# Optimization experiments

Measured on AMD Instinct MI355X. Metric: run time of the kernel, lower is better.

## Reference

```python
import jax, jax.numpy as jnp
import numpy as np

N, D, H, DH, DFF, E = 4096, 512, 8, 64, 2048, 65536


def setup_inputs() -> dict:
    key = jax.random.key(0)
    ks = jax.random.split(key, 20)
    g = lambda k, s: jax.random.normal(k, s, dtype=jnp.float32) * 0.02
    inp = {
        'x': jax.random.normal(ks[0], (N, D), dtype=jnp.float32),
        'edge_index': jax.random.randint(ks[1], (2, E), 0, N),
        'edge_attr': jax.random.uniform(ks[2], (E,), dtype=jnp.float32),
        'Wg': g(ks[3], (D, D)), 'bg': jnp.zeros((D,), jnp.float32),
        'ln1_s': jnp.ones((D,), jnp.float32), 'ln1_b': jnp.zeros((D,), jnp.float32),
        'Wq': g(ks[4], (D, D)), 'bq': jnp.zeros((D,), jnp.float32),
        'Wk': g(ks[5], (D, D)), 'bk': jnp.zeros((D,), jnp.float32),
        'Wv': g(ks[6], (D, D)), 'bv': jnp.zeros((D,), jnp.float32),
        'Wo': g(ks[7], (D, D)), 'bo': jnp.zeros((D,), jnp.float32),
        'ln2_s': jnp.ones((D,), jnp.float32), 'ln2_b': jnp.zeros((D,), jnp.float32),
        'W1': g(ks[8], (D, DFF)), 'b1': jnp.zeros((DFF,), jnp.float32),
        'W2': g(ks[9], (DFF, D)), 'b2': jnp.zeros((D,), jnp.float32),
        'Wa': g(ks[10], (2 * D, D)), 'ba': jnp.zeros((D,), jnp.float32),
    }
    return inp


def _ln(x, s, b):
    m = x.mean(-1, keepdims=True)
    v = ((x - m) ** 2).mean(-1, keepdims=True)
    return (x - m) * jax.lax.rsqrt(v + 1e-5) * s + b


def _gcn(x, edge_index, ew, Wg, bg):
    # GCNConv: linear, add self-loops (weight 1), sym deg normalization, scatter-add
    xt = x @ Wg                                   # [N, D]
    src = jnp.concatenate([edge_index[0], jnp.arange(N)])
    dst = jnp.concatenate([edge_index[1], jnp.arange(N)])
    w = jnp.concatenate([ew, jnp.ones((N,), ew.dtype)])
    deg = jax.ops.segment_sum(w, dst, num_segments=N)
    dinv = jnp.where(deg > 0, jax.lax.rsqrt(jnp.maximum(deg, 1e-12)), 0.0)
    coef = dinv[src] * w * dinv[dst]              # [E+N]
    out = jax.ops.segment_sum(xt[src] * coef[:, None], dst, num_segments=N)
    return out + bg


def _tfm(x, p):
    # pre-LN vanilla transformer block over all N nodes as one sequence
    h = _ln(x, p['ln1_s'], p['ln1_b'])
    q = (h @ p['Wq'] + p['bq']).reshape(N, H, DH)
    k = (h @ p['Wk'] + p['bk']).reshape(N, H, DH)
    v = (h @ p['Wv'] + p['bv']).reshape(N, H, DH)
    scores = jnp.einsum('nhd,mhd->hnm', q, k) / np.sqrt(DH)
    a = jax.nn.softmax(scores, axis=-1)
    o = jnp.einsum('hnm,mhd->nhd', a, v).reshape(N, D)
    x = x + o @ p['Wo'] + p['bo']
    h2 = _ln(x, p['ln2_s'], p['ln2_b'])
    mlp = jax.nn.gelu(h2 @ p['W1'] + p['b1']) @ p['W2'] + p['b2']
    return x + mlp


def reference(x, edge_index, edge_attr, Wg, bg, ln1_s, ln1_b, Wq, bq, Wk, bk, Wv, bv,
              Wo, bo, ln2_s, ln2_b, W1, b1, W2, b2, Wa, ba):
    p = dict(ln1_s=ln1_s, ln1_b=ln1_b, Wq=Wq, bq=bq, Wk=Wk, bk=bk, Wv=Wv, bv=bv,
             Wo=Wo, bo=bo, ln2_s=ln2_s, ln2_b=ln2_b, W1=W1, b1=b1, W2=W2, b2=b2)
    mp = _gcn(x, edge_index, edge_attr, Wg, bg)
    tf = _tfm(x, p)
    return x + jnp.concatenate([mp, tf], axis=-1) @ Wa + ba
```

## Files before the change

### kernel.cpp

```cpp
#include <hip/hip_runtime.h>
#include <math.h>

#define N_NODES 4096
#define DMODEL  512
#define NHEAD   8
#define DHEAD   64
#define DFF     2048
#define NEDGE   65536
#define QKVLD   1536

typedef unsigned short u16;
typedef __bf16 bf16x8 __attribute__((ext_vector_type(8)));
typedef float  f32x4  __attribute__((ext_vector_type(4)));
typedef short  s16x4  __attribute__((ext_vector_type(4)));

#if defined(__has_builtin)
#if __has_builtin(__builtin_amdgcn_mfma_f32_16x16x16bf16_1k)
#define HAS_MFMA_1K 1
#endif
#endif

__device__ inline float fast_exp2(float x) {
    return __builtin_amdgcn_exp2f(x);
}

__device__ inline f32x4 mfma16(bf16x8 a, bf16x8 b, f32x4 c) {
    return __builtin_amdgcn_mfma_f32_16x16x32_bf16(a, b, c, 0, 0, 0);
}

#ifdef HAS_MFMA_1K
__device__ inline f32x4 mfma1k(s16x4 a, s16x4 b, f32x4 c) {
    return __builtin_amdgcn_mfma_f32_16x16x16bf16_1k(a, b, c, 0, 0, 0);
}
__device__ inline s16x4 pack_bf4(f32x4 p) {
    union { float f; unsigned u; } a0, a1, a2, a3;
    a0.f = p[0]; a1.f = p[1]; a2.f = p[2]; a3.f = p[3];
    unsigned lo = __builtin_amdgcn_perm(a1.u + 0x8000u, a0.u + 0x8000u, 0x07060302u);
    unsigned hi = __builtin_amdgcn_perm(a3.u + 0x8000u, a2.u + 0x8000u, 0x07060302u);
    union { unsigned u[2]; s16x4 v; } r;
    r.u[0] = lo; r.u[1] = hi;
    return r.v;
}
#endif

__device__ inline u16 f2bf(float f) {
    union { float f; unsigned u; } v; v.f = f;
    unsigned r = v.u + 0x7fff + ((v.u >> 16) & 1);
    return (u16)(r >> 16);
}

__device__ inline float bf2f(u16 v) {
    union { unsigned u; float f; } t; t.u = ((unsigned)v) << 16; return t.f;
}

__device__ inline float gelu_tanh(float x) {
    float x3 = x * x * x;
    float t = tanhf(0.7978845608028654f * (x + 0.044715f * x3));
    return 0.5f * x * (1.0f + t);
}

#define GBN 128
#define GBK 32
#define GP  40

template <int ACT, int OBF16>
__launch_bounds__(512)
__global__ void mfma_gemm64(const u16* __restrict__ A, const u16* __restrict__ Bt,
                            const float* __restrict__ bias, const float* __restrict__ res,
                            void* __restrict__ Cout, int M, int Nn, int K, float scale,
                            int ldC, int ldRes) {
    __shared__ u16 Asm[2][64 * GP];
    __shared__ u16 Bsm[2][128 * GP];

    const int tid = threadIdx.x;
    const int w = tid >> 6;
    const int lane = tid & 63;
    const int quad = lane >> 4;
    const int l15 = lane & 15;
    const int row0 = blockIdx.y * 64;
    const int col0 = blockIdx.x * GBN;
    const int rh = (w & 1) * 32;
    const int cg = (w >> 1) * 32;

    f32x4 acc[2][2];
#pragma unroll
    for (int i = 0; i < 2; ++i)
#pragma unroll
        for (int j = 0; j < 2; ++j) acc[i][j] = (f32x4){0.f, 0.f, 0.f, 0.f};

    const int brow = tid >> 2, bk = (tid & 3) * 8;
    const int arow = (tid & 255) >> 2, ak = (tid & 3) * 8;
    const bool doA = (tid < 256);

    {
        uint4 b0 = *(const uint4*)&Bt[(size_t)(col0 + brow) * K + bk];
        *(uint4*)&Bsm[0][brow * GP + bk] = b0;
        if (doA) {
            uint4 a0 = *(const uint4*)&A[(size_t)(row0 + arow) * K + ak];
            *(uint4*)&Asm[0][arow * GP + ak] = a0;
        }
    }
    __syncthreads();

    const int nT = K / GBK;
    for (int t = 0; t < nT; ++t) {
        const int buf = t & 1;
        uint4 an, bn;
        if (t + 1 < nT) {
            const int k0 = (t + 1) * GBK;
            bn = *(const uint4*)&Bt[(size_t)(col0 + brow) * K + k0 + bk];
            if (doA) an = *(const uint4*)&A[(size_t)(row0 + arow) * K + k0 + ak];
        }
        bf16x8 af[2], bf[2];
#pragma unroll
        for (int i = 0; i < 2; ++i)
            af[i] = *(const bf16x8*)&Asm[buf][(rh + i * 16 + l15) * GP + quad * 8];
#pragma unroll
        for (int j = 0; j < 2; ++j)
            bf[j] = *(const bf16x8*)&Bsm[buf][(cg + j * 16 + l15) * GP + quad * 8];
#pragma unroll
        for (int i = 0; i < 2; ++i)
#pragma unroll
            for (int j = 0; j < 2; ++j)
                acc[i][j] = mfma16(af[i], bf[j], acc[i][j]);
        if (t + 1 < nT) {
            *(uint4*)&Bsm[buf ^ 1][brow * GP + bk] = bn;
            if (doA) *(uint4*)&Asm[buf ^ 1][arow * GP + ak] = an;
            __syncthreads();
        }
    }

#pragma unroll
    for (int j = 0; j < 2; ++j) {
        const int col = col0 + cg + j * 16 + l15;
        const float bc = bias ? bias[col] : 0.f;
#pragma unroll
        for (int i = 0; i < 2; ++i) {
#pragma unroll
            for (int r = 0; r < 4; ++r) {
                const int row = row0 + rh + i * 16 + quad * 4 + r;
                float o = (acc[i][j][r] + bc) * scale;
                if (ACT == 1) o = gelu_tanh(o);
                if (res) o += res[(size_t)row * ldRes + col];
                if (OBF16)
                    ((u16*)Cout)[(size_t)row * ldC + col] = f2bf(o);
                else
                    ((float*)Cout)[(size_t)row * ldC + col] = o;
            }
        }
    }
}

#define QSCALE 0.1803368801111204f

__launch_bounds__(256)
__global__ void qkvg_gemm(const u16* __restrict__ xb, const u16* __restrict__ hb,
                          const u16* __restrict__ Wall,
                          const float* __restrict__ bq, const float* __restrict__ bk,
                          const float* __restrict__ bv,
                          u16* __restrict__ xtb, u16* __restrict__ qkvb,
                          u16* __restrict__ vtb) {
    __shared__ u16 Asm[2][64 * GP];
    __shared__ u16 Bsm[2][128 * GP];

    const int tid = threadIdx.x;
    const int w = tid >> 6;
    const int lane = tid & 63;
    const int quad = lane >> 4;
    const int l15 = lane & 15;
    const int row0 = blockIdx.y * 64;
    const int col0 = blockIdx.x * GBN;
    const int wn = w * 32;
    const int K = DMODEL;
    const u16* A = (col0 < 512) ? xb : hb;

    f32x4 acc[4][2];
#pragma unroll
    for (int i = 0; i < 4; ++i)
#pragma unroll
        for (int j = 0; j < 2; ++j) acc[i][j] = (f32x4){0.f, 0.f, 0.f, 0.f};

    const int c1 = tid, c2 = tid + 256;
    const int ar1 = c1 >> 2, ak1 = (c1 & 3) * 8;
    const int ar2 = c2 >> 2, ak2 = (c2 & 3) * 8;

    {
        uint4 a0 = *(const uint4*)&A   [(size_t)(row0 + ar1) * K + ak1];
        uint4 b0 = *(const uint4*)&Wall[(size_t)(col0 + ar1) * K + ak1];
        uint4 b1 = *(const uint4*)&Wall[(size_t)(col0 + ar2) * K + ak2];
        *(uint4*)&Asm[0][ar1 * GP + ak1] = a0;
        *(uint4*)&Bsm[0][ar1 * GP + ak1] = b0;
        *(uint4*)&Bsm[0][ar2 * GP + ak2] = b1;
    }
    __syncthreads();

    const int nT = K / GBK;
    for (int t = 0; t < nT; ++t) {
        const int buf = t & 1;
        uint4 an, bn0, bn1;
        if (t + 1 < nT) {
            const int k0 = (t + 1) * GBK;
            an  = *(const uint4*)&A   [(size_t)(row0 + ar1) * K + k0 + ak1];
            bn0 = *(const uint4*)&Wall[(size_t)(col0 + ar1) * K + k0 + ak1];
            bn1 = *(const uint4*)&Wall[(size_t)(col0 + ar2) * K + k0 + ak2];
        }
        bf16x8 af[4], bf[2];
#pragma unroll
        for (int i = 0; i < 4; ++i)
            af[i] = *(const bf16x8*)&Asm[buf][(i * 16 + l15) * GP + quad * 8];
#pragma unroll
        for (int j = 0; j < 2; ++j)
            bf[j] = *(const bf16x8*)&Bsm[buf][(wn + j * 16 + l15) * GP + quad * 8];
#pragma unroll
        for (int i = 0; i < 4; ++i)
#pragma unroll
            for (int j = 0; j < 2; ++j)
                acc[i][j] = mfma16(af[i], bf[j], acc[i][j]);
        if (t + 1 < nT) {
            *(uint4*)&Asm[buf ^ 1][ar1 * GP + ak1] = an;
            *(uint4*)&Bsm[buf ^ 1][ar1 * GP + ak1] = bn0;
            *(uint4*)&Bsm[buf ^ 1][ar2 * GP + ak2] = bn1;
            __syncthreads();
        }
    }

#pragma unroll
    for (int j = 0; j < 2; ++j) {
        const int col = col0 + wn + j * 16 + l15;
        if (col < 512) {
#pragma unroll
            for (int i = 0; i < 4; ++i)
#pragma unroll
                for (int r = 0; r < 4; ++r)
                    xtb[(size_t)(row0 + i * 16 + quad * 4 + r) * 512 + col] =
                        f2bf(acc[i][j][r]);
        } else if (col < 1536) {
            const float bc = (col < 1024) ? bq[col - 512] : bk[col - 1024];
            const float scale = (col < 1024) ? QSCALE : 1.0f;
#pragma unroll
            for (int i = 0; i < 4; ++i)
#pragma unroll
                for (int r = 0; r < 4; ++r)
                    qkvb[(size_t)(row0 + i * 16 + quad * 4 + r) * QKVLD + col - 512] =
                        f2bf((acc[i][j][r] + bc) * scale);
        } else {
            const int hd = col - 1536;
            const float bc = bv[hd];
#pragma unroll
            for (int i = 0; i < 4; ++i) {
                ushort4 pk;
                pk.x = f2bf(acc[i][j][0] + bc);
                pk.y = f2bf(acc[i][j][1] + bc);
                pk.z = f2bf(acc[i][j][2] + bc);
                pk.w = f2bf(acc[i][j][3] + bc);
                *(uint2*)&vtb[(size_t)hd * N_NODES + row0 + i * 16 + quad * 4] =
                    *(uint2*)&pk;
            }
        }
    }
}

__device__ inline float block_sum_256(float v, float* red4) {
#pragma unroll
    for (int o = 32; o > 0; o >>= 1) v += __shfl_down(v, o, 64);
    const int lane = threadIdx.x & 63;
    const int w = threadIdx.x >> 6;
    if (lane == 0) red4[w] = v;
    __syncthreads();
    return red4[0] + red4[1] + red4[2] + red4[3];
}

__launch_bounds__(256)
__global__ void prep_kernel(
    const float* __restrict__ Wg, const float* __restrict__ Wq,
    const float* __restrict__ Wk, const float* __restrict__ Wv,
    const float* __restrict__ Wo, const float* __restrict__ W1,
    const float* __restrict__ W2, const float* __restrict__ Wa,
    u16* __restrict__ Wgt, u16* __restrict__ Wqt, u16* __restrict__ Wkt,
    u16* __restrict__ Wvt, u16* __restrict__ Wot, u16* __restrict__ W1t,
    u16* __restrict__ W2t, u16* __restrict__ Wat,
    const float* __restrict__ x, u16* __restrict__ xb,
    const float* __restrict__ ln1s, const float* __restrict__ ln1b,
    u16* __restrict__ hb, float* __restrict__ deg, int* __restrict__ cnt) {
    __shared__ u16 t[32][34];
    __shared__ float redA[4];
    __shared__ float redB[4];
    const int id = blockIdx.x;

    if (id < 3840) {
        const float* W; u16* Wt; int K, Nn, bx, by;
        if (id < 1280) {
            const int m = id >> 8, tt = id & 255;
            bx = tt & 15; by = tt >> 4; K = 512; Nn = 512;
            W  = (m == 0) ? Wg  : (m == 1) ? Wq  : (m == 2) ? Wk  : (m == 3) ? Wv  : Wo;
            Wt = (m == 0) ? Wgt : (m == 1) ? Wqt : (m == 2) ? Wkt : (m == 3) ? Wvt : Wot;
        } else if (id < 2304) {
            const int tt = id - 1280; bx = tt & 63; by = tt >> 6;
            K = 512; Nn = 2048; W = W1; Wt = W1t;
        } else if (id < 3328) {
            const int tt = id - 2304; bx = tt & 15; by = tt >> 4;
            K = 2048; Nn = 512; W = W2; Wt = W2t;
        } else {
            const int tt = id - 3328; bx = tt & 15; by = tt >> 4;
            K = 1024; Nn = 512; W = Wa; Wt = Wat;
        }
        const int k0 = by * 32, n0 = bx * 32;
        const int r = threadIdx.x >> 3, c4 = (threadIdx.x & 7) * 4;
        float4 v = *(const float4*)&W[(size_t)(k0 + r) * Nn + n0 + c4];
        t[r][c4 + 0] = f2bf(v.x); t[r][c4 + 1] = f2bf(v.y);
        t[r][c4 + 2] = f2bf(v.z); t[r][c4 + 3] = f2bf(v.w);
        __syncthreads();
        u16 tmp[4];
#pragma unroll
        for (int i = 0; i < 4; ++i) tmp[i] = t[c4 + i][r];
        u16* op = Wt + (size_t)(n0 + r) * K + k0 + c4;
        *(uint2*)op = *(uint2*)tmp;
    } else if (id < 5888) {
        size_t i = ((size_t)(id - 3840) * 256 + threadIdx.x) * 4;
        float4 v = *(const float4*)&x[i];
        ushort4 o;
        o.x = f2bf(v.x); o.y = f2bf(v.y); o.z = f2bf(v.z); o.w = f2bf(v.w);
        *(ushort4*)&xb[i] = o;
    } else if (id < 9984) {
        const int row = id - 5888;
        const int tid = threadIdx.x;
        const float* xr = x + (size_t)row * DMODEL;
        float v0 = xr[tid], v1 = xr[tid + 256];
        float total = block_sum_256(v0 + v1, redA);
        float mean = total * (1.0f / DMODEL);
        float d0 = v0 - mean, d1 = v1 - mean;
        float sq = block_sum_256(d0 * d0 + d1 * d1, redB);
        float inv = rsqrtf(sq * (1.0f / DMODEL) + 1e-5f);
        hb[(size_t)row * DMODEL + tid] = f2bf(d0 * inv * ln1s[tid] + ln1b[tid]);
        hb[(size_t)row * DMODEL + tid + 256] =
            f2bf(d1 * inv * ln1s[tid + 256] + ln1b[tid + 256]);
    } else {
        int i = (id - 9984) * 256 + threadIdx.x;
        deg[i] = 1.0f;
        cnt[i] = 0;
    }
}

__launch_bounds__(256)
__global__ void ln_kernel(const float* __restrict__ X, const float* __restrict__ s,
                          const float* __restrict__ b, u16* __restrict__ Y) {
    __shared__ float redA[4];
    __shared__ float redB[4];
    const int row = blockIdx.x;
    const int tid = threadIdx.x;
    const float* xr = X + (size_t)row * DMODEL;
    float v0 = xr[tid], v1 = xr[tid + 256];
    float total = block_sum_256(v0 + v1, redA);
    float mean = total * (1.0f / DMODEL);
    float d0 = v0 - mean, d1 = v1 - mean;
    float sq = block_sum_256(d0 * d0 + d1 * d1, redB);
    float inv = rsqrtf(sq * (1.0f / DMODEL) + 1e-5f);
    Y[(size_t)row * DMODEL + tid] = f2bf(d0 * inv * s[tid] + b[tid]);
    Y[(size_t)row * DMODEL + tid + 256] = f2bf(d1 * inv * s[tid + 256] + b[tid + 256]);
}

__global__ void gcn_count_kernel(const int* __restrict__ ei, const float* __restrict__ ew,
                                 float* __restrict__ deg, int* __restrict__ cnt) {
    int e = blockIdx.x * 256 + threadIdx.x;
    int d = ei[NEDGE + e];
    atomicAdd(&cnt[d], 1);
    atomicAdd(&deg[d], ew[e]);
}

__launch_bounds__(256)
__global__ void gcn_prefix_kernel(const int* __restrict__ cnt, int* __restrict__ off,
                                  int* __restrict__ cur, const float* __restrict__ deg,
                                  float* __restrict__ dinv) {
    __shared__ int part[256];
    const int tid = threadIdx.x;
    int local[16];
    int s = 0;
#pragma unroll
    for (int i = 0; i < 16; ++i) { local[i] = s; s += cnt[tid * 16 + i]; }
    part[tid] = s;
#pragma unroll
    for (int i = 0; i < 16; ++i) {
        const int n = tid * 16 + i;
        float d = deg[n];
        dinv[n] = (d > 0.f) ? rsqrtf(fmaxf(d, 1e-12f)) : 0.f;
    }
    __syncthreads();
    if (tid == 0) {
        int run = 0;
        for (int j = 0; j < 256; ++j) { int t = part[j]; part[j] = run; run += t; }
        off[N_NODES] = run;
    }
    __syncthreads();
    int p = part[tid];
#pragma unroll
    for (int i = 0; i < 16; ++i) {
        off[tid * 16 + i] = p + local[i];
        cur[tid * 16 + i] = p + local[i];
    }
}

__global__ void gcn_fill_kernel(const int* __restrict__ ei, const float* __restrict__ ew,
                                int* __restrict__ cur, int* __restrict__ esrc,
                                float* __restrict__ eww) {
    int e = blockIdx.x * 256 + threadIdx.x;
    int s = ei[e], d = ei[NEDGE + e];
    int pos = atomicAdd(&cur[d], 1);
    esrc[pos] = s;
    eww[pos] = ew[e];
}

__launch_bounds__(256)
__global__ void gcn_gather_kernel(const u16* __restrict__ xtb, const int* __restrict__ off,
                                  const int* __restrict__ esrc, const float* __restrict__ eww,
                                  const float* __restrict__ dinv, const float* __restrict__ bg,
                                  u16* __restrict__ catb) {
    const int d = blockIdx.x;
    const int b0 = off[d], b1 = off[d + 1];
    const float did = dinv[d];
    const int c = threadIdx.x * 2;
    float a0 = 0.f, a1 = 0.f;
    for (int j = b0; j < b1; ++j) {
        const int s = esrc[j];
        const float coef = dinv[s] * eww[j] * did;
        const unsigned pv = *(const unsigned*)&xtb[(size_t)s * DMODEL + c];
        a0 += coef * bf2f((u16)(pv & 0xffff));
        a1 += coef * bf2f((u16)(pv >> 16));
    }
    {
        const unsigned pv = *(const unsigned*)&xtb[(size_t)d * DMODEL + c];
        const float sl = did * did;
        a0 += sl * bf2f((u16)(pv & 0xffff));
        a1 += sl * bf2f((u16)(pv >> 16));
    }
    const unsigned pk = (unsigned)f2bf(a0 + bg[c]) | ((unsigned)f2bf(a1 + bg[c + 1]) << 16);
    *(unsigned*)&catb[(size_t)d * 1024 + c] = pk;
}

#define TK 64
#define AP 72
#define NSPLIT 8
#define KSPAN (N_NODES / NSPLIT)

__launch_bounds__(256)
__global__ void attn_kernel(const u16* __restrict__ Qkv, const u16* __restrict__ Vtb,
                            u16* __restrict__ Ob0, u16* __restrict__ Ob1,
                            u16* __restrict__ Ob2, u16* __restrict__ Ob3,
                            float* __restrict__ lpart) {
    __shared__ u16 Ks[64 * AP];
    __shared__ u16 Vs[64 * AP];
#ifndef HAS_MFMA_1K
    __shared__ u16 Ps[4][2][16 * AP];
#endif

    const int h = blockIdx.x;
    const int q0 = blockIdx.y * 128;
    const int sp = blockIdx.z;
    u16* bases0 = (sp < 2) ? Ob0 : (sp < 4) ? Ob1 : (sp < 6) ? Ob2 : Ob3;
    u16* __restrict__ Opx = bases0 + (size_t)(sp & 1) * N_NODES * DMODEL;
    const int kbase = sp * KSPAN;

    const int tid = threadIdx.x;
    const int w = tid >> 6;
    const int lane = tid & 63;
    const int quad = lane >> 4;
    const int l15 = lane & 15;

    const u16* qp = Qkv + (size_t)(q0 + w * 32 + l15) * QKVLD + h * DHEAD + quad * 8;
    bf16x8 qf[2][2];
    qf[0][0] = *(const bf16x8*)qp;
    qf[0][1] = *(const bf16x8*)(qp + 32);
    qf[1][0] = *(const bf16x8*)(qp + 16 * QKVLD);
    qf[1][1] = *(const bf16x8*)(qp + 16 * QKVLD + 32);

    f32x4 Oa[2][4];
#pragma unroll
    for (int a = 0; a < 2; ++a)
#pragma unroll
        for (int g = 0; g < 4; ++g) Oa[a][g] = (f32x4){0.f, 0.f, 0.f, 0.f};
    float ls[2] = {0.f, 0.f};

    const int srow = (tid & 127) >> 1;
    const int scol = (tid & 1) * 32;

    for (int kt = kbase; kt < kbase + KSPAN; kt += TK) {
        if (tid < 128) {
            const uint4* kg = (const uint4*)(Qkv + (size_t)(kt + srow) * QKVLD + 512 + h * DHEAD + scol);
            uint4* kd = (uint4*)&Ks[srow * AP + scol];
            kd[0] = kg[0]; kd[1] = kg[1]; kd[2] = kg[2]; kd[3] = kg[3];
        } else {
            const uint4* vg = (const uint4*)(Vtb + ((size_t)h * DHEAD + srow) * N_NODES + kt + scol);
            uint4* vd = (uint4*)&Vs[srow * AP + scol];
            vd[0] = vg[0]; vd[1] = vg[1]; vd[2] = vg[2]; vd[3] = vg[3];
        }
        __syncthreads();

        f32x4 St[2][4];
#pragma unroll
        for (int f = 0; f < 4; ++f) {
            const u16* kr = &Ks[(f * 16 + l15) * AP + quad * 8];
            bf16x8 k0 = *(const bf16x8*)kr;
            bf16x8 k1 = *(const bf16x8*)(kr + 32);
#pragma unroll
            for (int a = 0; a < 2; ++a) {
                f32x4 z = (f32x4){0.f, 0.f, 0.f, 0.f};
                z = mfma16(k0, qf[a][0], z);
                St[a][f] = mfma16(k1, qf[a][1], z);
            }
        }

#ifdef HAS_MFMA_1K
        s16x4 pk[2][4];
#pragma unroll
        for (int a = 0; a < 2; ++a)
#pragma unroll
            for (int f = 0; f < 4; ++f) {
                f32x4 p;
                p[0] = fast_exp2(St[a][f][0]);
                p[1] = fast_exp2(St[a][f][1]);
                p[2] = fast_exp2(St[a][f][2]);
                p[3] = fast_exp2(St[a][f][3]);
                ls[a] += (p[0] + p[1]) + (p[2] + p[3]);
                pk[a][f] = pack_bf4(p);
            }
#pragma unroll
        for (int f = 0; f < 4; ++f)
#pragma unroll
            for (int g = 0; g < 4; ++g) {
                const s16x4 vv = *(const s16x4*)&Vs[(g * 16 + l15) * AP + f * 16 + quad * 4];
                Oa[0][g] = mfma1k(pk[0][f], vv, Oa[0][g]);
                Oa[1][g] = mfma1k(pk[1][f], vv, Oa[1][g]);
            }
#else
        bf16x8 pa[2][2];
#pragma unroll
        for (int a = 0; a < 2; ++a) {
            u16* pw = Ps[w][a];
#pragma unroll
            for (int f = 0; f < 4; ++f) {
                float p0 = fast_exp2(St[a][f][0]);
                float p1 = fast_exp2(St[a][f][1]);
                float p2 = fast_exp2(St[a][f][2]);
                float p3 = fast_exp2(St[a][f][3]);
                ls[a] += (p0 + p1) + (p2 + p3);
                ushort4 pkk;
                pkk.x = f2bf(p0); pkk.y = f2bf(p1); pkk.z = f2bf(p2); pkk.w = f2bf(p3);
                *(uint2*)&pw[l15 * AP + f * 16 + quad * 4] = *(uint2*)&pkk;
            }
            const u16* pr = &pw[l15 * AP + quad * 8];
            pa[a][0] = *(const bf16x8*)pr;
            pa[a][1] = *(const bf16x8*)(pr + 32);
        }
#pragma unroll
        for (int g = 0; g < 4; ++g) {
            const u16* vr = &Vs[(g * 16 + l15) * AP + quad * 8];
            bf16x8 v0 = *(const bf16x8*)vr;
            bf16x8 v1 = *(const bf16x8*)(vr + 32);
#pragma unroll
            for (int a = 0; a < 2; ++a) {
                Oa[a][g] = mfma16(pa[a][0], v0, Oa[a][g]);
                Oa[a][g] = mfma16(pa[a][1], v1, Oa[a][g]);
            }
        }
#endif
        __syncthreads();
    }

#pragma unroll
    for (int a = 0; a < 2; ++a) {
        float s = ls[a];
        s += __shfl_xor(s, 16, 64);
        s += __shfl_xor(s, 32, 64);
        const int rowbase = q0 + w * 32 + a * 16;
        if (quad == 0)
            lpart[(size_t)(sp * NHEAD + h) * N_NODES + rowbase + l15] = s;
#pragma unroll
        for (int r = 0; r < 4; ++r) {
            u16* op = Opx + (size_t)(rowbase + quad * 4 + r) * DMODEL + h * DHEAD + l15;
#pragma unroll
            for (int g = 0; g < 4; ++g) op[g * 16] = f2bf(Oa[a][g][r]);
        }
    }
}

__global__ void attn_reduce_kernel(const u16* __restrict__ Ob0, const u16* __restrict__ Ob1,
                                   const u16* __restrict__ Ob2, const u16* __restrict__ Ob3,
                                   const float* __restrict__ lpart, u16* __restrict__ attb) {
    size_t i4 = ((size_t)blockIdx.x * 256 + threadIdx.x) * 4;
    const int row = (int)(i4 >> 9);
    const int h = ((int)i4 & 511) >> 6;
    const size_t OFF = (size_t)N_NODES * DMODEL;
    const u16* bases[4] = {Ob0, Ob1, Ob2, Ob3};
    float s0 = 0.f, s1 = 0.f, s2 = 0.f, s3 = 0.f;
#pragma unroll
    for (int b = 0; b < 4; ++b)
#pragma unroll
        for (int k = 0; k < 2; ++k) {
            uint2 v = *(const uint2*)(bases[b] + k * OFF + i4);
            s0 += bf2f((u16)(v.x & 0xffff)); s1 += bf2f((u16)(v.x >> 16));
            s2 += bf2f((u16)(v.y & 0xffff)); s3 += bf2f((u16)(v.y >> 16));
        }
    const float* lp = lpart + (size_t)h * N_NODES + row;
    const size_t S = (size_t)NHEAD * N_NODES;
    float l = 0.f;
#pragma unroll
    for (int sp = 0; sp < NSPLIT; ++sp) l += lp[sp * S];
    const float inv = 1.0f / l;
    ushort4 r;
    r.x = f2bf(s0 * inv); r.y = f2bf(s1 * inv);
    r.z = f2bf(s2 * inv); r.w = f2bf(s3 * inv);
    *(ushort4*)&attb[i4] = r;
}

static void mgemm64(hipStream_t st, const u16* A, const u16* Bt, const float* bias,
                    const float* res, void* C, int M, int Nn, int K, float scale,
                    int act, int obf16, int ldC, int ldRes) {
    dim3 g(Nn / GBN, M / 64), b(512);
    if (act)
        hipLaunchKernelGGL((mfma_gemm64<1, 1>), g, b, 0, st, A, Bt, bias, res, C, M, Nn, K, scale, ldC, ldRes);
    else if (obf16)
        hipLaunchKernelGGL((mfma_gemm64<0, 1>), g, b, 0, st, A, Bt, bias, res, C, M, Nn, K, scale, ldC, ldRes);
    else
        hipLaunchKernelGGL((mfma_gemm64<0, 0>), g, b, 0, st, A, Bt, bias, res, C, M, Nn, K, scale, ldC, ldRes);
}

extern "C" void kernel_launch(void* const* d_in, const int* in_sizes, int n_in,
                              void* d_out, int out_size, void* d_ws, size_t ws_size,
                              hipStream_t stream) {
    const float* x    = (const float*)d_in[0];
    const int*   ei   = (const int*)d_in[1];
    const float* ew   = (const float*)d_in[2];
    const float* Wg   = (const float*)d_in[3];
    const float* bg   = (const float*)d_in[4];
    const float* ln1s = (const float*)d_in[5];
    const float* ln1b = (const float*)d_in[6];
    const float* Wq   = (const float*)d_in[7];
    const float* bq   = (const float*)d_in[8];
    const float* Wk   = (const float*)d_in[9];
    const float* bk   = (const float*)d_in[10];
    const float* Wv   = (const float*)d_in[11];
    const float* bv   = (const float*)d_in[12];
    const float* Wo   = (const float*)d_in[13];
    const float* bo   = (const float*)d_in[14];
    const float* ln2s = (const float*)d_in[15];
    const float* ln2b = (const float*)d_in[16];
    const float* W1   = (const float*)d_in[17];
    const float* b1   = (const float*)d_in[18];
    const float* W2   = (const float*)d_in[19];
    const float* b2   = (const float*)d_in[20];
    const float* Wa   = (const float*)d_in[21];
    const float* ba   = (const float*)d_in[22];
    float* out = (float*)d_out;
    float* ws  = (float*)d_ws;

    const size_t SLOT = (size_t)N_NODES * DMODEL;

    u16*   xtb = (u16*)ws;
    u16*   Ob0 = (u16*)ws;
    float* x1  = ws;
    float* lpart = ws + SLOT;
    int*   esrc  = (int*)(ws + SLOT + 327680);
    float* eww   = (float*)(esrc + NEDGE);
    int*   off   = (int*)(eww + NEDGE);
    int*   cur   = off + 4100;
    int*   cnt   = cur + 4096;
    u16* Ob1 = (u16*)(ws + 2 * SLOT);
    u16* hb   = (u16*)(ws + 3 * SLOT);
    u16* attb = hb + SLOT;
    u16* h2b  = hb + SLOT;
    u16* qkvb = (u16*)(ws + 4 * SLOT);
    u16* vtb  = (u16*)(ws + 5 * SLOT) + SLOT;
    u16* Ob2  = (u16*)(ws + 6 * SLOT);
    u16* Ob3  = (u16*)(ws + 7 * SLOT);
    u16* midb = (u16*)(ws + 6 * SLOT);
    u16* catb = (u16*)(ws + 8 * SLOT);
    u16* xb   = catb;
    u16* Wgt = (u16*)(ws + 9 * SLOT);
    u16* Wqt = Wgt + 262144;
    u16* Wkt = Wqt + 262144;
    u16* Wvt = Wkt + 262144;
    u16* Wot = Wvt + 262144;
    u16* W1t = Wot + 262144;
    u16* W2t = W1t + 1048576;
    u16* Wat = W2t + 1048576;
    float* deg  = (float*)(Wat + 524288);
    float* dinv = deg + N_NODES;

    hipLaunchKernelGGL(prep_kernel, dim3(10000), dim3(256), 0, stream,
                       Wg, Wq, Wk, Wv, Wo, W1, W2, Wa,
                       Wgt, Wqt, Wkt, Wvt, Wot, W1t, W2t, Wat,
                       x, xb, ln1s, ln1b, hb, deg, cnt);

    hipLaunchKernelGGL(qkvg_gemm, dim3(16, 64), dim3(256), 0, stream,
                       xb, hb, Wgt, bq, bk, bv, xtb, qkvb, vtb);

    hipLaunchKernelGGL(gcn_count_kernel, dim3(NEDGE / 256), dim3(256), 0, stream, ei, ew, deg, cnt);
    hipLaunchKernelGGL(gcn_prefix_kernel, dim3(1), dim3(256), 0, stream, cnt, off, cur, deg, dinv);
    hipLaunchKernelGGL(gcn_fill_kernel, dim3(NEDGE / 256), dim3(256), 0, stream, ei, ew, cur, esrc, eww);
    hipLaunchKernelGGL(gcn_gather_kernel, dim3(N_NODES), dim3(256), 0, stream,
                       xtb, off, esrc, eww, dinv, bg, catb);

    hipLaunchKernelGGL(attn_kernel, dim3(NHEAD, N_NODES / 128, NSPLIT), dim3(256), 0, stream,
                       qkvb, vtb, Ob0, Ob1, Ob2, Ob3, lpart);
    hipLaunchKernelGGL(attn_reduce_kernel, dim3((int)(SLOT / 1024)), dim3(256), 0, stream,
                       Ob0, Ob1, Ob2, Ob3, lpart, attb);

    mgemm64(stream, attb, Wot, bo, x, x1, N_NODES, DMODEL, DMODEL, 1.0f, 0, 0, DMODEL, DMODEL);
    hipLaunchKernelGGL(ln_kernel, dim3(N_NODES), dim3(256), 0, stream, x1, ln2s, ln2b, h2b);
    mgemm64(stream, h2b, W1t, b1, nullptr, midb, N_NODES, DFF, DMODEL, 1.0f, 1, 1, DFF, DFF);
    mgemm64(stream, midb, W2t, b2, x1, catb + 512, N_NODES, DMODEL, DFF, 1.0f, 0, 1, 1024, DMODEL);

    mgemm64(stream, catb, Wat, ba, x, out, N_NODES, DMODEL, 2 * DMODEL, 1.0f, 0, 0, DMODEL, DMODEL);
}
```

Before: 340.6 us.

## Fuse attention split-reduction into Wo GEMM A-tile load and merge x cast into LN1

```diff
diff --git a/kernel.cpp b/kernel.cpp
--- a/kernel.cpp
+++ b/kernel.cpp
@@ -146,6 +146,135 @@
                     ((u16*)Cout)[(size_t)row * ldC + col] = f2bf(o);
                 else
                     ((float*)Cout)[(size_t)row * ldC + col] = o;
+            }
+        }
+    }
+}
+
+__device__ inline uint4 reduce8_norm(const u16* b0, const u16* b1, const u16* b2,
+                                     const u16* b3, size_t off, float linv) {
+    const size_t OFF = (size_t)N_NODES * DMODEL;
+    float s[8] = {0.f, 0.f, 0.f, 0.f, 0.f, 0.f, 0.f, 0.f};
+    const u16* bs[4] = {b0, b1, b2, b3};
+#pragma unroll
+    for (int b = 0; b < 4; ++b)
+#pragma unroll
+        for (int k = 0; k < 2; ++k) {
+            uint4 v = *(const uint4*)(bs[b] + k * OFF + off);
+            unsigned uu[4] = {v.x, v.y, v.z, v.w};
+#pragma unroll
+            for (int t = 0; t < 4; ++t) {
+                s[2 * t]     += bf2f((u16)(uu[t] & 0xffff));
+                s[2 * t + 1] += bf2f((u16)(uu[t] >> 16));
+            }
+        }
+    uint4 r;
+    r.x = (unsigned)f2bf(s[0] * linv) | ((unsigned)f2bf(s[1] * linv) << 16);
+    r.y = (unsigned)f2bf(s[2] * linv) | ((unsigned)f2bf(s[3] * linv) << 16);
+    r.z = (unsigned)f2bf(s[4] * linv) | ((unsigned)f2bf(s[5] * linv) << 16);
+    r.w = (unsigned)f2bf(s[6] * linv) | ((unsigned)f2bf(s[7] * linv) << 16);
+    return r;
+}
+
+__launch_bounds__(512)
+__global__ void wo_gemm(const u16* __restrict__ Ob0, const u16* __restrict__ Ob1,
+                        const u16* __restrict__ Ob2, const u16* __restrict__ Ob3,
+                        const float* __restrict__ lpart, const u16* __restrict__ Bt,
+                        const float* __restrict__ bias, const float* __restrict__ res,
+                        float* __restrict__ Cout) {
+    __shared__ u16 Asm[2][64 * GP];
+    __shared__ u16 Bsm[2][128 * GP];
+
+    const int tid = threadIdx.x;
+    const int w = tid >> 6;
+    const int lane = tid & 63;
+    const int quad = lane >> 4;
+    const int l15 = lane & 15;
+    const int row0 = blockIdx.y * 64;
+    const int col0 = blockIdx.x * GBN;
+    const int rh = (w & 1) * 32;
+    const int cg = (w >> 1) * 32;
+    const int K = DMODEL;
+
+    f32x4 acc[2][2];
+#pragma unroll
+    for (int i = 0; i < 2; ++i)
+#pragma unroll
+        for (int j = 0; j < 2; ++j) acc[i][j] = (f32x4){0.f, 0.f, 0.f, 0.f};
+
+    const int brow = tid >> 2, bk = (tid & 3) * 8;
+    const int arow = (tid & 255) >> 2, ak = (tid & 3) * 8;
+    const bool doA = (tid < 256);
+
+    float linv[8];
+    if (doA) {
+        const float* lr = lpart + (size_t)(row0 + arow) * 64;
+        float ls[8] = {0.f, 0.f, 0.f, 0.f, 0.f, 0.f, 0.f, 0.f};
+#pragma unroll
+        for (int v = 0; v < 16; ++v) {
+            float4 q = *(const float4*)&lr[v * 4];
+            ls[(v * 4 + 0) & 7] += q.x;
+            ls[(v * 4 + 1) & 7] += q.y;
+            ls[(v * 4 + 2) & 7] += q.z;
+            ls[(v * 4 + 3) & 7] += q.w;
+        }
+#pragma unroll
+        for (int hh = 0; hh < 8; ++hh) linv[hh] = 1.0f / ls[hh];
+    }
+
+    {
+        uint4 b0 = *(const uint4*)&Bt[(size_t)(col0 + brow) * K + bk];
+        *(uint4*)&Bsm[0][brow * GP + bk] = b0;
+        if (doA) {
+            uint4 a0 = reduce8_norm(Ob0, Ob1, Ob2, Ob3,
+                                    (size_t)(row0 + arow) * DMODEL + ak, linv[0]);
+            *(uint4*)&Asm[0][arow * GP + ak] = a0;
+        }
+    }
+    __syncthreads();
+
+#pragma unroll
+    for (int t = 0; t < 16; ++t) {
+        const int buf = t & 1;
+        uint4 an, bn;
+        if (t + 1 < 16) {
+            const int k0 = (t + 1) * GBK;
+            bn = *(const uint4*)&Bt[(size_t)(col0 + brow) * K + k0 + bk];
+            if (doA)
+                an = reduce8_norm(Ob0, Ob1, Ob2, Ob3,
+                                  (size_t)(row0 + arow) * DMODEL + k0 + ak,
+                                  linv[(t + 1) >> 1]);
+        }
+        bf16x8 af[2], bf[2];
+#pragma unroll
+        for (int i = 0; i < 2; ++i)
+            af[i] = *(const bf16x8*)&Asm[buf][(rh + i * 16 + l15) * GP + quad * 8];
+#pragma unroll
+        for (int j = 0; j < 2; ++j)
+            bf[j] = *(const bf16x8*)&Bsm[buf][(cg + j * 16 + l15) * GP + quad * 8];
+#pragma unroll
+        for (int i = 0; i < 2; ++i)
+#pragma unroll
+            for (int j = 0; j < 2; ++j)
+                acc[i][j] = mfma16(af[i], bf[j], acc[i][j]);
+        if (t + 1 < 16) {
+            *(uint4*)&Bsm[buf ^ 1][brow * GP + bk] = bn;
+            if (doA) *(uint4*)&Asm[buf ^ 1][arow * GP + ak] = an;
+            __syncthreads();
+        }
+    }
+
+#pragma unroll
+    for (int j = 0; j < 2; ++j) {
+        const int col = col0 + cg + j * 16 + l15;
+        const float bc = bias[col];
+#pragma unroll
+        for (int i = 0; i < 2; ++i) {
+#pragma unroll
+            for (int r = 0; r < 4; ++r) {
+                const int row = row0 + rh + i * 16 + quad * 4 + r;
+                Cout[(size_t)row * DMODEL + col] =
+                    acc[i][j][r] + bc + res[(size_t)row * DMODEL + col];
             }
         }
     }
@@ -315,17 +444,13 @@
         for (int i = 0; i < 4; ++i) tmp[i] = t[c4 + i][r];
         u16* op = Wt + (size_t)(n0 + r) * K + k0 + c4;
         *(uint2*)op = *(uint2*)tmp;
-    } else if (id < 5888) {
-        size_t i = ((size_t)(id - 3840) * 256 + threadIdx.x) * 4;
-        float4 v = *(const float4*)&x[i];
-        ushort4 o;
-        o.x = f2bf(v.x); o.y = f2bf(v.y); o.z = f2bf(v.z); o.w = f2bf(v.w);
-        *(ushort4*)&xb[i] = o;
-    } else if (id < 9984) {
-        const int row = id - 5888;
+    } else if (id < 7936) {
+        const int row = id - 3840;
         const int tid = threadIdx.x;
         const float* xr = x + (size_t)row * DMODEL;
         float v0 = xr[tid], v1 = xr[tid + 256];
+        xb[(size_t)row * DMODEL + tid] = f2bf(v0);
+        xb[(size_t)row * DMODEL + tid + 256] = f2bf(v1);
         float total = block_sum_256(v0 + v1, redA);
         float mean = total * (1.0f / DMODEL);
         float d0 = v0 - mean, d1 = v1 - mean;
@@ -335,7 +460,7 @@
         hb[(size_t)row * DMODEL + tid + 256] =
             f2bf(d1 * inv * ln1s[tid + 256] + ln1b[tid + 256]);
     } else {
-        int i = (id - 9984) * 256 + threadIdx.x;
+        int i = (id - 7936) * 256 + threadIdx.x;
         deg[i] = 1.0f;
         cnt[i] = 0;
     }
@@ -572,7 +697,7 @@
         s += __shfl_xor(s, 32, 64);
         const int rowbase = q0 + w * 32 + a * 16;
         if (quad == 0)
-            lpart[(size_t)(sp * NHEAD + h) * N_NODES + rowbase + l15] = s;
+            lpart[(size_t)(rowbase + l15) * 64 + sp * 8 + h] = s;
 #pragma unroll
         for (int r = 0; r < 4; ++r) {
             u16* op = Opx + (size_t)(rowbase + quad * 4 + r) * DMODEL + h * DHEAD + l15;
@@ -580,35 +705,6 @@
             for (int g = 0; g < 4; ++g) op[g * 16] = f2bf(Oa[a][g][r]);
         }
     }
-}
-
-__global__ void attn_reduce_kernel(const u16* __restrict__ Ob0, const u16* __restrict__ Ob1,
-                                   const u16* __restrict__ Ob2, const u16* __restrict__ Ob3,
-                                   const float* __restrict__ lpart, u16* __restrict__ attb) {
-    size_t i4 = ((size_t)blockIdx.x * 256 + threadIdx.x) * 4;
-    const int row = (int)(i4 >> 9);
-    const int h = ((int)i4 & 511) >> 6;
-    const size_t OFF = (size_t)N_NODES * DMODEL;
-    const u16* bases[4] = {Ob0, Ob1, Ob2, Ob3};
-    float s0 = 0.f, s1 = 0.f, s2 = 0.f, s3 = 0.f;
-#pragma unroll
-    for (int b = 0; b < 4; ++b)
-#pragma unroll
-        for (int k = 0; k < 2; ++k) {
-            uint2 v = *(const uint2*)(bases[b] + k * OFF + i4);
-            s0 += bf2f((u16)(v.x & 0xffff)); s1 += bf2f((u16)(v.x >> 16));
-            s2 += bf2f((u16)(v.y & 0xffff)); s3 += bf2f((u16)(v.y >> 16));
-        }
-    const float* lp = lpart + (size_t)h * N_NODES + row;
-    const size_t S = (size_t)NHEAD * N_NODES;
-    float l = 0.f;
-#pragma unroll
-    for (int sp = 0; sp < NSPLIT; ++sp) l += lp[sp * S];
-    const float inv = 1.0f / l;
-    ushort4 r;
-    r.x = f2bf(s0 * inv); r.y = f2bf(s1 * inv);
-    r.z = f2bf(s2 * inv); r.w = f2bf(s3 * inv);
-    *(ushort4*)&attb[i4] = r;
 }
 
 static void mgemm64(hipStream_t st, const u16* A, const u16* Bt, const float* bias,
@@ -654,9 +750,8 @@
 
     const size_t SLOT = (size_t)N_NODES * DMODEL;
 
-    u16*   xtb = (u16*)ws;
-    u16*   Ob0 = (u16*)ws;
-    float* x1  = ws;
+    u16* xtb = (u16*)ws;
+    u16* Ob0 = (u16*)ws;
     float* lpart = ws + SLOT;
     int*   esrc  = (int*)(ws + SLOT + 327680);
     float* eww   = (float*)(esrc + NEDGE);
@@ -664,11 +759,11 @@
     int*   cur   = off + 4100;
     int*   cnt   = cur + 4096;
     u16* Ob1 = (u16*)(ws + 2 * SLOT);
-    u16* hb   = (u16*)(ws + 3 * SLOT);
-    u16* attb = hb + SLOT;
-    u16* h2b  = hb + SLOT;
-    u16* qkvb = (u16*)(ws + 4 * SLOT);
-    u16* vtb  = (u16*)(ws + 5 * SLOT) + SLOT;
+    u16* hb  = (u16*)(ws + 3 * SLOT);
+    u16* h2b = hb + SLOT;
+    u16*   qkvb = (u16*)(ws + 4 * SLOT);
+    float* x1   = ws + 4 * SLOT;
+    u16*   vtb  = (u16*)(ws + 5 * SLOT) + SLOT;
     u16* Ob2  = (u16*)(ws + 6 * SLOT);
     u16* Ob3  = (u16*)(ws + 7 * SLOT);
     u16* midb = (u16*)(ws + 6 * SLOT);
@@ -685,7 +780,7 @@
     float* deg  = (float*)(Wat + 524288);
     float* dinv = deg + N_NODES;
 
-    hipLaunchKernelGGL(prep_kernel, dim3(10000), dim3(256), 0, stream,
+    hipLaunchKernelGGL(prep_kernel, dim3(7952), dim3(256), 0, stream,
                        Wg, Wq, Wk, Wv, Wo, W1, W2, Wa,
                        Wgt, Wqt, Wkt, Wvt, Wot, W1t, W2t, Wat,
                        x, xb, ln1s, ln1b, hb, deg, cnt);
@@ -701,10 +796,10 @@
 
     hipLaunchKernelGGL(attn_kernel, dim3(NHEAD, N_NODES / 128, NSPLIT), dim3(256), 0, stream,
                        qkvb, vtb, Ob0, Ob1, Ob2, Ob3, lpart);
-    hipLaunchKernelGGL(attn_reduce_kernel, dim3((int)(SLOT / 1024)), dim3(256), 0, stream,
-                       Ob0, Ob1, Ob2, Ob3, lpart, attb);
-
-    mgemm64(stream, attb, Wot, bo, x, x1, N_NODES, DMODEL, DMODEL, 1.0f, 0, 0, DMODEL, DMODEL);
+
+    hipLaunchKernelGGL(wo_gemm, dim3(4, 64), dim3(512), 0, stream,
+                       Ob0, Ob1, Ob2, Ob3, lpart, Wot, bo, x, x1);
+
     hipLaunchKernelGGL(ln_kernel, dim3(N_NODES), dim3(256), 0, stream, x1, ln2s, ln2b, h2b);
     mgemm64(stream, h2b, W1t, b1, nullptr, midb, N_NODES, DFF, DMODEL, 1.0f, 1, 1, DFF, DFF);
     mgemm64(stream, midb, W2t, b2, x1, catb + 512, N_NODES, DMODEL, DFF, 1.0f, 0, 1, 1024, DMODEL);
```

Measured after the change: 336.1 us. About the same (-1.3%).
